# Performance work log

Hardware: AMD Instinct MI355X
Metric: run time of the kernel (lower is better)

The kernel has to match this reference:

```python
import jax, jax.numpy as jnp
import numpy as np

N = 100000   # nodes
E = 6400000  # edges
D = 3        # manifold / gauge dim (number of kernels)
ORDER = 2    # number of gradient layers
HID = 256
OUT = 64


def setup_inputs() -> dict:
    key = jax.random.key(0)
    ks = jax.random.split(key, 8)
    x = jax.random.normal(ks[0], (N, D), dtype=jnp.float32)
    gauges = jax.random.normal(ks[1], (N, D, D), dtype=jnp.float32)
    kernel_vals = jax.random.normal(ks[2], (D, E), dtype=jnp.float32)
    feat_in = D + D * D + D * D * D  # 39
    W1 = jax.random.normal(ks[3], (feat_in, HID), dtype=jnp.float32) * 0.1
    b1 = jax.random.normal(ks[4], (HID,), dtype=jnp.float32) * 0.1
    W2 = jax.random.normal(ks[5], (HID, OUT), dtype=jnp.float32) * 0.1
    b2 = jax.random.normal(ks[6], (OUT,), dtype=jnp.float32) * 0.1
    edge_index = jax.random.randint(ks[7], (2, E), 0, N, dtype=jnp.int64)
    return {"x": x, "gauges": gauges, "kernel_vals": kernel_vals,
            "W1": W1, "b1": b1, "W2": W2, "b2": b2,
            "edge_index": edge_index}


def _aniso_conv(x, src, dst, kernel_vals):
    # x: [N, c]; kernel_vals: [D, E]. out[v] = sum_e K[k,e] * x[src[e]] at dst[e]
    xs = x[src]  # [E, c] gathered once, reused across kernels
    outs = []
    for k in range(kernel_vals.shape[0]):  # small fixed set of D kernels
        m = kernel_vals[k][:, None] * xs  # [E, c]
        outs.append(jax.ops.segment_sum(m, dst, num_segments=N))
    out = jnp.stack(outs, axis=2)  # [N, c, D] (matches torch.stack(axis=2))
    return out.reshape(N, -1)      # [N, c*D]


def reference(x, gauges, kernel_vals, W1, b1, W2, b2, edge_index):
    # map signal to local gauges: project x onto gauge columns
    xl = jnp.einsum("nji,nj->ni", gauges, x)  # [N, D]
    src, dst = edge_index[0], edge_index[1]
    out = [xl]
    h = xl
    for _ in range(ORDER):
        h = _aniso_conv(h, src, dst, kernel_vals)
        out.append(h)
    feats = jnp.concatenate(out, axis=1)  # [N, D + D^2 + D^3]
    # encoder MLP
    hmid = jax.nn.relu(feats @ W1 + b1)
    emb = hmid @ W2 + b2
    return emb
```

## Files before the change

### kernel.cpp

```cpp
#include <hip/hip_runtime.h>

#define N_NODES 100000
#define N_EDGES 6400000
#define FEAT 39
#define HID 256
#define OUT 64
#define NB 8

#define NBKT  2000
#define BKN   50
#define NSETS 8
#define PAD1  640
#define P1_WGS 1024
#define EPW1  (N_EDGES / P1_WGS)
#define ORD_STRIDE (NSETS * PAD1)

#define OFF_XL   0
#define OFF_H1   ((size_t)N_NODES * 16)
#define OFF_H2   (OFF_H1 + (size_t)N_NODES * 48)
#define OFF_CUR  (OFF_H2 + (size_t)N_NODES * 112)
#define OFF_PFXG ((OFF_CUR + (size_t)NSETS * NBKT * 4 + 255) & ~(size_t)255)
#define OFF_ORDG ((OFF_PFXG + (size_t)NBKT * 64 * 4 + 255) & ~(size_t)255)
#define OFF_STR  ((OFF_ORDG + (size_t)NBKT * ORD_STRIDE * 2 + 255) & ~(size_t)255)
#define WS_SORT_NEEDED (OFF_STR + (size_t)NSETS * NBKT * PAD1 * 16)

__global__ void xl_kernel(const float* __restrict__ x,
                          const float* __restrict__ gauges,
                          float* __restrict__ xl) {
    int n = blockIdx.x * blockDim.x + threadIdx.x;
    if (n >= N_NODES) return;
    float x0 = x[n * 3 + 0], x1 = x[n * 3 + 1], x2 = x[n * 3 + 2];
    const float* g = gauges + n * 9;
    float4 o;
    o.x = g[0] * x0 + g[3] * x1 + g[6] * x2;
    o.y = g[1] * x0 + g[4] * x1 + g[7] * x2;
    o.z = g[2] * x0 + g[5] * x1 + g[8] * x2;
    o.w = 0.f;
    ((float4*)xl)[n] = o;
}

__global__ __launch_bounds__(256) void bin_kernel(const int* __restrict__ ei,
                                                  const float* __restrict__ kv,
                                                  int* __restrict__ cur,
                                                  float4* __restrict__ strips) {
    int w = blockIdx.x, t = threadIdx.x;
    int s;
    asm volatile("s_getreg_b32 %0, hwreg(HW_REG_XCC_ID)" : "=s"(s));
    s &= (NSETS - 1);
    int e0 = w * EPW1;
    for (int e = e0 + t; e < e0 + EPW1; e += 256) {
        int src = ei[e];
        int d   = ei[N_EDGES + e];
        int b   = d / BKN;
        int dl  = d - b * BKN;
        float4 p;
        p.x = kv[e];
        p.y = kv[N_EDGES + e];
        p.z = kv[2 * N_EDGES + e];
        p.w = __int_as_float(src | (dl << 17));
        int cell = s * NBKT + b;
        int slot = atomicAdd(&cur[cell], 1);
        if (slot < PAD1) strips[(size_t)cell * PAD1 + slot] = p;
    }
}

__global__ __launch_bounds__(256) void conv1_sort(const int* __restrict__ cur,
                                                  const float4* __restrict__ strips,
                                                  const float4* __restrict__ xl,
                                                  float* __restrict__ h1,
                                                  unsigned short* __restrict__ ord_g,
                                                  int* __restrict__ pfx_g) {
    __shared__ int segpfx[NSETS + 1];
    __shared__ int ncnt[BKN];
    __shared__ int npfx[BKN + 1];
    __shared__ int ncur[BKN];
    __shared__ unsigned tmp[ORD_STRIDE];
    __shared__ unsigned short ord[ORD_STRIDE];
    int b = blockIdx.x, t = threadIdx.x;

    for (int i = t; i < BKN; i += 256) ncnt[i] = 0;
    if (t == 0) {
        int run = 0;
        for (int s = 0; s < NSETS; ++s) {
            segpfx[s] = run;
            int c = cur[s * NBKT + b];
            run += (c < PAD1 ? c : PAD1);
        }
        segpfx[NSETS] = run;
    }
    __syncthreads();
    int total = segpfx[NSETS];

    for (int j = t; j < total; j += 256) {
        int s = 0;
#pragma unroll
        for (int k = 1; k < NSETS; ++k) s += (j >= segpfx[k]);
        int idx = j - segpfx[s];
        const float* cell = (const float*)&strips[((size_t)(s * NBKT + b)) * PAD1 + idx];
        unsigned pw = __float_as_uint(cell[3]);
        int dl = (pw >> 17) & 63;
        atomicAdd(&ncnt[dl], 1);
        tmp[j] = ((unsigned)dl << 16) | ((unsigned)s << 10) | (unsigned)idx;
    }
    __syncthreads();
    if (t == 0) {
        int run = 0;
        for (int i = 0; i < BKN; ++i) { npfx[i] = run; ncur[i] = run; run += ncnt[i]; }
        npfx[BKN] = run;
    }
    __syncthreads();
    for (int j = t; j < total; j += 256) {
        unsigned v = tmp[j];
        int slot = atomicAdd(&ncur[v >> 16], 1);
        ord[slot] = (unsigned short)(v & 0xFFFF);
    }
    __syncthreads();
    for (int j = t; j < total; j += 256) ord_g[(size_t)b * ORD_STRIDE + j] = ord[j];
    for (int i = t; i <= BKN; i += 256) pfx_g[b * 64 + i] = npfx[i];

    int wave = t >> 6, lane = t & 63;
    for (int n = wave; n < BKN; n += 4) {
        int st = npfx[n], en = npfx[n + 1];
        float a[9];
#pragma unroll
        for (int c = 0; c < 9; ++c) a[c] = 0.f;
        for (int i = st + lane; i < en; i += 64) {
            unsigned short v = ord[i];
            int s = v >> 10, idx = v & 1023;
            float4 p = strips[((size_t)(s * NBKT + b)) * PAD1 + idx];
            float4 xs = xl[__float_as_uint(p.w) & 0x1FFFF];
            a[0] += p.x * xs.x; a[1] += p.y * xs.x; a[2] += p.z * xs.x;
            a[3] += p.x * xs.y; a[4] += p.y * xs.y; a[5] += p.z * xs.y;
            a[6] += p.x * xs.z; a[7] += p.y * xs.z; a[8] += p.z * xs.z;
        }
#pragma unroll
        for (int off = 32; off > 0; off >>= 1) {
#pragma unroll
            for (int c = 0; c < 9; ++c) a[c] += __shfl_xor(a[c], off, 64);
        }
        if (lane == 0) {
            float* r = h1 + (size_t)(b * BKN + n) * 12;
            ((float4*)r)[0] = make_float4(a[0], a[1], a[2], a[3]);
            ((float4*)r)[1] = make_float4(a[4], a[5], a[6], a[7]);
            ((float4*)r)[2] = make_float4(a[8], 0.f, 0.f, 0.f);
        }
    }
}

__global__ __launch_bounds__(256) void conv2_sort(const float4* __restrict__ strips,
                                                  const float* __restrict__ h1,
                                                  float* __restrict__ h2,
                                                  const unsigned short* __restrict__ ord_g,
                                                  const int* __restrict__ pfx_g) {
    __shared__ int npfx[BKN + 1];
    int b = blockIdx.x, t = threadIdx.x;
    for (int i = t; i <= BKN; i += 256) npfx[i] = pfx_g[b * 64 + i];
    __syncthreads();
    const unsigned short* ob = ord_g + (size_t)b * ORD_STRIDE;
    int wave = t >> 6, lane = t & 63;
    for (int n = wave; n < BKN; n += 4) {
        int st = npfx[n], en = npfx[n + 1];
        float a[27];
#pragma unroll
        for (int c = 0; c < 27; ++c) a[c] = 0.f;
        for (int i = st + lane; i < en; i += 64) {
            unsigned short v = ob[i];
            int s = v >> 10, idx = v & 1023;
            float4 p = strips[((size_t)(s * NBKT + b)) * PAD1 + idx];
            int src = __float_as_uint(p.w) & 0x1FFFF;
            const float4* hs = (const float4*)(h1 + (size_t)src * 12);
            float4 v0 = hs[0], v1 = hs[1], v2 = hs[2];
            float h[9] = {v0.x, v0.y, v0.z, v0.w, v1.x, v1.y, v1.z, v1.w, v2.x};
#pragma unroll
            for (int c = 0; c < 9; ++c) {
                a[c * 3 + 0] += p.x * h[c];
                a[c * 3 + 1] += p.y * h[c];
                a[c * 3 + 2] += p.z * h[c];
            }
        }
#pragma unroll
        for (int off = 32; off > 0; off >>= 1) {
#pragma unroll
            for (int c = 0; c < 27; ++c) a[c] += __shfl_xor(a[c], off, 64);
        }
        if (lane == 0) {
            float* r = h2 + (size_t)(b * BKN + n) * 28;
#pragma unroll
            for (int q = 0; q < 6; ++q)
                ((float4*)r)[q] = make_float4(a[q*4], a[q*4+1], a[q*4+2], a[q*4+3]);
            ((float4*)r)[6] = make_float4(a[24], a[25], a[26], 0.f);
        }
    }
}

__global__ void edge1_atomic(const int* __restrict__ ei,
                             const float* __restrict__ kv,
                             const float* __restrict__ xl,
                             float* __restrict__ h1) {
    int e = blockIdx.x * blockDim.x + threadIdx.x;
    if (e >= N_EDGES) return;
    int s = ei[e], d = ei[N_EDGES + e];
    float k0 = kv[e], k1 = kv[N_EDGES + e], k2 = kv[2 * N_EDGES + e];
    const float* xs = xl + (size_t)s * 4;
    float* hd = h1 + (size_t)d * 12;
#pragma unroll
    for (int c = 0; c < 3; ++c) {
        float v = xs[c];
        atomicAdd(hd + c * 3 + 0, k0 * v);
        atomicAdd(hd + c * 3 + 1, k1 * v);
        atomicAdd(hd + c * 3 + 2, k2 * v);
    }
}

__global__ void edge2_atomic(const int* __restrict__ ei,
                             const float* __restrict__ kv,
                             const float* __restrict__ h1,
                             float* __restrict__ h2) {
    int e = blockIdx.x * blockDim.x + threadIdx.x;
    if (e >= N_EDGES) return;
    int s = ei[e], d = ei[N_EDGES + e];
    float k0 = kv[e], k1 = kv[N_EDGES + e], k2 = kv[2 * N_EDGES + e];
    const float* hs = h1 + (size_t)s * 12;
    float* hd = h2 + (size_t)d * 28;
#pragma unroll
    for (int c = 0; c < 9; ++c) {
        float v = hs[c];
        atomicAdd(hd + c * 3 + 0, k0 * v);
        atomicAdd(hd + c * 3 + 1, k1 * v);
        atomicAdd(hd + c * 3 + 2, k2 * v);
    }
}

__global__ __launch_bounds__(256) void mlp_kernel(const float* __restrict__ xl,
                                                  const float* __restrict__ h1,
                                                  const float* __restrict__ h2,
                                                  const float* __restrict__ W1,
                                                  const float* __restrict__ b1,
                                                  const float* __restrict__ W2,
                                                  const float* __restrict__ b2,
                                                  float* __restrict__ out) {
    __shared__ float f[NB][FEAT + 1];
    __shared__ float hmid[NB][HID];
    __shared__ float partial[4][NB][OUT];

    int t = threadIdx.x;
    int base = blockIdx.x * NB;

    for (int i = t; i < NB * FEAT; i += 256) {
        int m = i / FEAT, k = i % FEAT;
        int n = base + m;
        float v = 0.f;
        if (n < N_NODES) {
            if (k < 3)       v = xl[(size_t)n * 4 + k];
            else if (k < 12) v = h1[(size_t)n * 12 + (k - 3)];
            else             v = h2[(size_t)n * 28 + (k - 12)];
        }
        f[m][k] = v;
    }
    __syncthreads();

    float acc[NB];
    float bb = b1[t];
#pragma unroll
    for (int m = 0; m < NB; ++m) acc[m] = bb;
#pragma unroll
    for (int k = 0; k < FEAT; ++k) {
        float w = W1[k * HID + t];
#pragma unroll
        for (int m = 0; m < NB; ++m) acc[m] += f[m][k] * w;
    }
#pragma unroll
    for (int m = 0; m < NB; ++m) hmid[m][t] = fmaxf(acc[m], 0.f);
    __syncthreads();

    int o = t & 63, q = t >> 6;
    float p[NB];
#pragma unroll
    for (int m = 0; m < NB; ++m) p[m] = 0.f;
    for (int hh = 0; hh < 64; ++hh) {
        int h = q * 64 + hh;
        float w = W2[h * OUT + o];
#pragma unroll
        for (int m = 0; m < NB; ++m) p[m] += hmid[m][h] * w;
    }
#pragma unroll
    for (int m = 0; m < NB; ++m) partial[q][m][o] = p[m];
    __syncthreads();

    if (t < OUT) {
        float bo = b2[t];
        for (int m = 0; m < NB; ++m) {
            int n = base + m;
            if (n < N_NODES) {
                out[n * OUT + t] = partial[0][m][t] + partial[1][m][t] +
                                   partial[2][m][t] + partial[3][m][t] + bo;
            }
        }
    }
}

extern "C" void kernel_launch(void* const* d_in, const int* in_sizes, int n_in,
                              void* d_out, int out_size, void* d_ws, size_t ws_size,
                              hipStream_t stream) {
    const float* x      = (const float*)d_in[0];
    const float* gauges = (const float*)d_in[1];
    const float* kv     = (const float*)d_in[2];
    const float* W1     = (const float*)d_in[3];
    const float* b1     = (const float*)d_in[4];
    const float* W2     = (const float*)d_in[5];
    const float* b2     = (const float*)d_in[6];
    const int*   ei     = (const int*)d_in[7];
    float* out = (float*)d_out;

    char* ws = (char*)d_ws;
    float* xl = (float*)(ws + OFF_XL);
    float* h1 = (float*)(ws + OFF_H1);
    float* h2 = (float*)(ws + OFF_H2);

    const int EB = (N_EDGES + 255) / 256;

    xl_kernel<<<(N_NODES + 255) / 256, 256, 0, stream>>>(x, gauges, xl);

    if (ws_size >= WS_SORT_NEEDED) {
        int*            cur   = (int*)(ws + OFF_CUR);
        int*            pfx_g = (int*)(ws + OFF_PFXG);
        unsigned short* ord_g = (unsigned short*)(ws + OFF_ORDG);
        float4*         strips = (float4*)(ws + OFF_STR);
        hipMemsetAsync(cur, 0, (size_t)NSETS * NBKT * 4, stream);
        bin_kernel<<<P1_WGS, 256, 0, stream>>>(ei, kv, cur, strips);
        conv1_sort<<<NBKT, 256, 0, stream>>>(cur, strips, (const float4*)xl, h1, ord_g, pfx_g);
        conv2_sort<<<NBKT, 256, 0, stream>>>(strips, h1, h2, ord_g, pfx_g);
    } else {
        hipMemsetAsync(h1, 0, (size_t)N_NODES * (48 + 112), stream);
        edge1_atomic<<<EB, 256, 0, stream>>>(ei, kv, xl, h1);
        edge2_atomic<<<EB, 256, 0, stream>>>(ei, kv, h1, h2);
    }

    mlp_kernel<<<(N_NODES + NB - 1) / NB, 256, 0, stream>>>(xl, h1, h2, W1, b1, W2, b2, out);
}
```

Baseline: 805.8 us.

## Split sort from convolution and use one thread per node for aggregation

Moves the per-bucket sort into its own kernel and replaces the wave-per-node aggregation in both convolution passes with a flat one-thread-per-node loop over that node's sorted edges. This removes the 64-lane shuffle reductions, which are costly for 27 accumulators while each node has only about 64 edges. In exchange, each thread walks its edges serially, so loads across a wavefront become scattered and uncoalesced, and per-thread latency grows. It also doubles the number of binning workgroups.

```diff
diff --git a/kernel.cpp b/kernel.cpp
--- a/kernel.cpp
+++ b/kernel.cpp
@@ -11,7 +11,7 @@
 #define BKN   50
 #define NSETS 8
 #define PAD1  640
-#define P1_WGS 1024
+#define P1_WGS 2048
 #define EPW1  (N_EDGES / P1_WGS)
 #define ORD_STRIDE (NSETS * PAD1)
 
@@ -64,12 +64,10 @@
     }
 }
 
-__global__ __launch_bounds__(256) void conv1_sort(const int* __restrict__ cur,
-                                                  const float4* __restrict__ strips,
-                                                  const float4* __restrict__ xl,
-                                                  float* __restrict__ h1,
-                                                  unsigned short* __restrict__ ord_g,
-                                                  int* __restrict__ pfx_g) {
+__global__ __launch_bounds__(256) void sort_kernel(const int* __restrict__ cur,
+                                                   const float4* __restrict__ strips,
+                                                   unsigned short* __restrict__ ord_g,
+                                                   int* __restrict__ pfx_g) {
     __shared__ int segpfx[NSETS + 1];
     __shared__ int ncnt[BKN];
     __shared__ int npfx[BKN + 1];
@@ -117,80 +115,69 @@
     __syncthreads();
     for (int j = t; j < total; j += 256) ord_g[(size_t)b * ORD_STRIDE + j] = ord[j];
     for (int i = t; i <= BKN; i += 256) pfx_g[b * 64 + i] = npfx[i];
-
-    int wave = t >> 6, lane = t & 63;
-    for (int n = wave; n < BKN; n += 4) {
-        int st = npfx[n], en = npfx[n + 1];
-        float a[9];
-#pragma unroll
-        for (int c = 0; c < 9; ++c) a[c] = 0.f;
-        for (int i = st + lane; i < en; i += 64) {
-            unsigned short v = ord[i];
-            int s = v >> 10, idx = v & 1023;
-            float4 p = strips[((size_t)(s * NBKT + b)) * PAD1 + idx];
-            float4 xs = xl[__float_as_uint(p.w) & 0x1FFFF];
-            a[0] += p.x * xs.x; a[1] += p.y * xs.x; a[2] += p.z * xs.x;
-            a[3] += p.x * xs.y; a[4] += p.y * xs.y; a[5] += p.z * xs.y;
-            a[6] += p.x * xs.z; a[7] += p.y * xs.z; a[8] += p.z * xs.z;
-        }
-#pragma unroll
-        for (int off = 32; off > 0; off >>= 1) {
-#pragma unroll
-            for (int c = 0; c < 9; ++c) a[c] += __shfl_xor(a[c], off, 64);
-        }
-        if (lane == 0) {
-            float* r = h1 + (size_t)(b * BKN + n) * 12;
-            ((float4*)r)[0] = make_float4(a[0], a[1], a[2], a[3]);
-            ((float4*)r)[1] = make_float4(a[4], a[5], a[6], a[7]);
-            ((float4*)r)[2] = make_float4(a[8], 0.f, 0.f, 0.f);
-        }
-    }
-}
-
-__global__ __launch_bounds__(256) void conv2_sort(const float4* __restrict__ strips,
+}
+
+__global__ __launch_bounds__(256) void conv1_flat(const float4* __restrict__ strips,
+                                                  const float4* __restrict__ xl,
+                                                  float* __restrict__ h1,
+                                                  const unsigned short* __restrict__ ord_g,
+                                                  const int* __restrict__ pfx_g) {
+    int n = blockIdx.x * blockDim.x + threadIdx.x;
+    if (n >= N_NODES) return;
+    int b = n / BKN, dl = n - b * BKN;
+    int st = pfx_g[b * 64 + dl], en = pfx_g[b * 64 + dl + 1];
+    const unsigned short* ob = ord_g + (size_t)b * ORD_STRIDE;
+    float a[9];
+#pragma unroll
+    for (int c = 0; c < 9; ++c) a[c] = 0.f;
+    for (int i = st; i < en; ++i) {
+        unsigned short v = ob[i];
+        int s = v >> 10, idx = v & 1023;
+        float4 p = strips[((size_t)(s * NBKT + b)) * PAD1 + idx];
+        float4 xs = xl[__float_as_uint(p.w) & 0x1FFFF];
+        a[0] += p.x * xs.x; a[1] += p.y * xs.x; a[2] += p.z * xs.x;
+        a[3] += p.x * xs.y; a[4] += p.y * xs.y; a[5] += p.z * xs.y;
+        a[6] += p.x * xs.z; a[7] += p.y * xs.z; a[8] += p.z * xs.z;
+    }
+    float* r = h1 + (size_t)n * 12;
+    ((float4*)r)[0] = make_float4(a[0], a[1], a[2], a[3]);
+    ((float4*)r)[1] = make_float4(a[4], a[5], a[6], a[7]);
+    ((float4*)r)[2] = make_float4(a[8], 0.f, 0.f, 0.f);
+}
+
+__global__ __launch_bounds__(256) void conv2_flat(const float4* __restrict__ strips,
                                                   const float* __restrict__ h1,
                                                   float* __restrict__ h2,
                                                   const unsigned short* __restrict__ ord_g,
                                                   const int* __restrict__ pfx_g) {
-    __shared__ int npfx[BKN + 1];
-    int b = blockIdx.x, t = threadIdx.x;
-    for (int i = t; i <= BKN; i += 256) npfx[i] = pfx_g[b * 64 + i];
-    __syncthreads();
+    int n = blockIdx.x * blockDim.x + threadIdx.x;
+    if (n >= N_NODES) return;
+    int b = n / BKN, dl = n - b * BKN;
+    int st = pfx_g[b * 64 + dl], en = pfx_g[b * 64 + dl + 1];
     const unsigned short* ob = ord_g + (size_t)b * ORD_STRIDE;
-    int wave = t >> 6, lane = t & 63;
-    for (int n = wave; n < BKN; n += 4) {
-        int st = npfx[n], en = npfx[n + 1];
-        float a[27];
-#pragma unroll
-        for (int c = 0; c < 27; ++c) a[c] = 0.f;
-        for (int i = st + lane; i < en; i += 64) {
-            unsigned short v = ob[i];
-            int s = v >> 10, idx = v & 1023;
-            float4 p = strips[((size_t)(s * NBKT + b)) * PAD1 + idx];
-            int src = __float_as_uint(p.w) & 0x1FFFF;
-            const float4* hs = (const float4*)(h1 + (size_t)src * 12);
-            float4 v0 = hs[0], v1 = hs[1], v2 = hs[2];
-            float h[9] = {v0.x, v0.y, v0.z, v0.w, v1.x, v1.y, v1.z, v1.w, v2.x};
-#pragma unroll
-            for (int c = 0; c < 9; ++c) {
-                a[c * 3 + 0] += p.x * h[c];
-                a[c * 3 + 1] += p.y * h[c];
-                a[c * 3 + 2] += p.z * h[c];
-            }
+    float a[27];
+#pragma unroll
+    for (int c = 0; c < 27; ++c) a[c] = 0.f;
+    for (int i = st; i < en; ++i) {
+        unsigned short v = ob[i];
+        int s = v >> 10, idx = v & 1023;
+        float4 p = strips[((size_t)(s * NBKT + b)) * PAD1 + idx];
+        int src = __float_as_uint(p.w) & 0x1FFFF;
+        const float4* hs = (const float4*)(h1 + (size_t)src * 12);
+        float4 v0 = hs[0], v1 = hs[1], v2 = hs[2];
+        float h[9] = {v0.x, v0.y, v0.z, v0.w, v1.x, v1.y, v1.z, v1.w, v2.x};
+#pragma unroll
+        for (int c = 0; c < 9; ++c) {
+            a[c * 3 + 0] += p.x * h[c];
+            a[c * 3 + 1] += p.y * h[c];
+            a[c * 3 + 2] += p.z * h[c];
         }
-#pragma unroll
-        for (int off = 32; off > 0; off >>= 1) {
-#pragma unroll
-            for (int c = 0; c < 27; ++c) a[c] += __shfl_xor(a[c], off, 64);
-        }
-        if (lane == 0) {
-            float* r = h2 + (size_t)(b * BKN + n) * 28;
-#pragma unroll
-            for (int q = 0; q < 6; ++q)
-                ((float4*)r)[q] = make_float4(a[q*4], a[q*4+1], a[q*4+2], a[q*4+3]);
-            ((float4*)r)[6] = make_float4(a[24], a[25], a[26], 0.f);
-        }
-    }
+    }
+    float* r = h2 + (size_t)n * 28;
+#pragma unroll
+    for (int q = 0; q < 6; ++q)
+        ((float4*)r)[q] = make_float4(a[q*4], a[q*4+1], a[q*4+2], a[q*4+3]);
+    ((float4*)r)[6] = make_float4(a[24], a[25], a[26], 0.f);
 }
 
 __global__ void edge1_atomic(const int* __restrict__ ei,
@@ -318,8 +305,9 @@
     float* h2 = (float*)(ws + OFF_H2);
 
     const int EB = (N_EDGES + 255) / 256;
-
-    xl_kernel<<<(N_NODES + 255) / 256, 256, 0, stream>>>(x, gauges, xl);
+    const int FB = (N_NODES + 255) / 256;
+
+    xl_kernel<<<FB, 256, 0, stream>>>(x, gauges, xl);
 
     if (ws_size >= WS_SORT_NEEDED) {
         int*            cur   = (int*)(ws + OFF_CUR);
@@ -328,8 +316,9 @@
         float4*         strips = (float4*)(ws + OFF_STR);
         hipMemsetAsync(cur, 0, (size_t)NSETS * NBKT * 4, stream);
         bin_kernel<<<P1_WGS, 256, 0, stream>>>(ei, kv, cur, strips);
-        conv1_sort<<<NBKT, 256, 0, stream>>>(cur, strips, (const float4*)xl, h1, ord_g, pfx_g);
-        conv2_sort<<<NBKT, 256, 0, stream>>>(strips, h1, h2, ord_g, pfx_g);
+        sort_kernel<<<NBKT, 256, 0, stream>>>(cur, strips, ord_g, pfx_g);
+        conv1_flat<<<FB, 256, 0, stream>>>(strips, (const float4*)xl, h1, ord_g, pfx_g);
+        conv2_flat<<<FB, 256, 0, stream>>>(strips, h1, h2, ord_g, pfx_g);
     } else {
         hipMemsetAsync(h1, 0, (size_t)N_NODES * (48 + 112), stream);
         edge1_atomic<<<EB, 256, 0, stream>>>(ei, kv, xl, h1);
```

Result: slower. 890.8 us (+10.6%).
